# Performance work log

Measured on AMD Instinct MI355X. Metric: run time of the kernel, lower is better.

## Reference

```python
import jax, jax.numpy as jnp
import numpy as np

B, T, H = 4, 2048, 1024
NH = 16
HD = H // NH  # 64
FF = 4 * H


def setup_inputs() -> dict:
    key = jax.random.key(0)
    ks = jax.random.split(key, 11)
    s = 0.02
    return {
        "x": jax.random.normal(ks[0], (B, T, H), dtype=jnp.float32),
        "Wq": jax.random.normal(ks[1], (H, H), dtype=jnp.float32) * s,
        "bq": jnp.zeros((H,), dtype=jnp.float32),
        "Wk": jax.random.normal(ks[2], (H, H), dtype=jnp.float32) * s,
        "bk": jnp.zeros((H,), dtype=jnp.float32),
        "Wv": jax.random.normal(ks[3], (H, H), dtype=jnp.float32) * s,
        "bv": jnp.zeros((H,), dtype=jnp.float32),
        "W1": jax.random.normal(ks[4], (H, FF), dtype=jnp.float32) * s,
        "b1": jnp.zeros((FF,), dtype=jnp.float32),
        "W2": jax.random.normal(ks[5], (FF, H), dtype=jnp.float32) * s,
        "b2": jnp.zeros((H,), dtype=jnp.float32),
    }


def _block(x, Wq, bq, Wk, bk, Wv, bv, W1, b1, W2, b2):
    b, t, h = x.shape
    # multi-head masked self-attention; NOTE: scale = full h_dim ** 0.5 (as in source)
    q = (x @ Wq + bq).reshape(b, t, NH, HD).transpose(0, 2, 1, 3)  # [B,nH,T,HD]
    k = (x @ Wk + bk).reshape(b, t, NH, HD).transpose(0, 2, 1, 3)
    v = (x @ Wv + bv).reshape(b, t, NH, HD).transpose(0, 2, 1, 3)
    att = jnp.einsum("bnqd,bnkd->bnqk", q, k) / (h ** 0.5)  # [B,nH,T,T]
    causal = jnp.tril(jnp.ones((t, t), dtype=bool))
    att = jnp.where(causal, att, -jnp.inf)
    w = jax.nn.softmax(att, axis=-1)
    attn_out = jnp.einsum("bnqk,bnkd->bnqd", w, v).transpose(0, 2, 1, 3).reshape(b, t, h)
    x = x + attn_out
    # MLP (dropout p=0 -> identity)
    mlp = jax.nn.gelu(x @ W1 + b1) @ W2 + b2
    return x + mlp


def reference(x, Wq, bq, Wk, bk, Wv, bv, W1, b1, W2, b2):
    return _block(x, Wq, bq, Wk, bk, Wv, bv, W1, b1, W2, b2)
```

## Files before the change

### kernel.cpp

```cpp
#include <hip/hip_runtime.h>
#include <cstdint>
#include <cstddef>

typedef unsigned short u16;
typedef __attribute__((ext_vector_type(8))) __bf16 bf16x8;
typedef __attribute__((ext_vector_type(4))) __bf16 bf16x4;
typedef __attribute__((ext_vector_type(4))) float f32x4;
typedef __attribute__((ext_vector_type(4))) u16 u16x4;

#define MFMA(a, b, c) __builtin_amdgcn_mfma_f32_16x16x32_bf16((a), (b), (c), 0, 0, 0)

__device__ __forceinline__ u16 f2b(float f) {
  union { __bf16 h; u16 u; } v;
  v.h = (__bf16)f;
  return v.u;
}

__device__ __forceinline__ void gld16(const void* g, void* l) {
  __builtin_amdgcn_global_load_lds(
      (__attribute__((address_space(1))) void*)(void*)(g),
      (__attribute__((address_space(3))) void*)(l), 16, 0, 0);
}

__device__ __forceinline__ size_t qk_off(int t, int hd) {
  return (size_t)((((t >> 4) * 2 + (hd >> 5)) * 512)
                  + ((((hd >> 3) & 3) * 16 + (t & 15)) * 8) + (hd & 7));
}
__device__ __forceinline__ size_t v_off(int t, int hd) {
  int kk = ((t & 15) << 2) | ((t >> 4) & 3);
  return (size_t)(((t >> 6) * 4096)
                  + (((hd >> 4) * 2 + (kk >> 5)) * 512)
                  + ((((kk >> 3) & 3) * 16 + (hd & 15)) * 8) + (kk & 7));
}

__global__ void xconv(const float* __restrict__ in, u16* __restrict__ out, int n) {
  int i = (blockIdx.x * blockDim.x + threadIdx.x) * 4;
  if (i >= n) return;
  float4 v = *(const float4*)(in + i);
  u16x4 o;
  o[0] = f2b(v.x); o[1] = f2b(v.y); o[2] = f2b(v.z); o[3] = f2b(v.w);
  *(u16x4*)(out + i) = o;
}

__global__ void wtrans_all(const float* __restrict__ Wq, const float* __restrict__ Wk,
                           const float* __restrict__ Wv, const float* __restrict__ W1,
                           const float* __restrict__ W2, u16* __restrict__ Wqkvt,
                           u16* __restrict__ W1t, u16* __restrict__ W2t) {
  __shared__ float tile[32][33];
  int blk = blockIdx.x;
  const float* W;
  u16* Wt;
  int Kd, Nd, nx;
  if (blk < 3072) {
    int s = blk >> 10;
    blk &= 1023;
    W = (s == 0) ? Wq : (s == 1) ? Wk : Wv;
    Wt = Wqkvt + (size_t)s * 1048576;
    Kd = 1024; Nd = 1024; nx = 32;
  } else if (blk < 7168) {
    blk -= 3072; W = W1; Wt = W1t; Kd = 1024; Nd = 4096; nx = 128;
  } else {
    blk -= 7168; W = W2; Wt = W2t; Kd = 4096; Nd = 1024; nx = 32;
  }
  int n0 = (blk % nx) * 32, k0 = (blk / nx) * 32;
  int tx = threadIdx.x, ty = threadIdx.y;
#pragma unroll
  for (int i = 0; i < 4; i++)
    tile[ty + i * 8][tx] = W[(size_t)(k0 + ty + i * 8) * Nd + n0 + tx];
  __syncthreads();
#pragma unroll
  for (int i = 0; i < 4; i++)
    Wt[(size_t)(n0 + ty + i * 8) * Kd + k0 + tx] = f2b(tile[tx][ty + i * 8]);
}

template <int MODE, int NW>
__global__ __launch_bounds__(NW * 64) void gemm_bt(
    const u16* __restrict__ A, const u16* __restrict__ Bt,
    const float* __restrict__ b0, const float* __restrict__ b1,
    const float* __restrict__ b2, void* __restrict__ outp,
    const float* __restrict__ resid, int N, int K, float scale) {
  constexpr int NT = NW * 64;
  constexpr int NTILE = (NW == 4) ? 4 : 2;
  __shared__ __attribute__((aligned(16))) u16 As[128 * 64];
  __shared__ __attribute__((aligned(16))) u16 Bs[128 * 64];
  const int tid = threadIdx.x;
  const int wid = tid >> 6, lane = tid & 63;
  const int g = lane >> 4, r = lane & 15;
  const int bm = blockIdx.y, bn = blockIdx.x;
  const int wrow = (NW == 4) ? (wid >> 1) * 64 : (wid >> 2) * 64;
  const int wcol = (NW == 4) ? (wid & 1) * 64 : (wid & 3) * 32;

  const f32x4 zero4 = {0.f, 0.f, 0.f, 0.f};
  f32x4 acc[4][NTILE];
#pragma unroll
  for (int i = 0; i < 4; i++)
#pragma unroll
    for (int j = 0; j < NTILE; j++) acc[i][j] = zero4;

  const size_t aBase = (size_t)bm * 128 * K;
  const size_t bBase = (size_t)bn * 128 * K;
  const int ko0 = ((0 * 4 + g) ^ (r & 7)) * 8;
  const int ko1 = ((1 * 4 + g) ^ (r & 7)) * 8;

  for (int k0 = 0; k0 < K; k0 += 64) {
    __syncthreads();
#pragma unroll
    for (int i = 0; i < 2048 / NT; i++) {
      const int c0 = i * NT;
      const int cc = (c0 + tid) & 1023;
      const int row = cc >> 3;
      const int js = ((cc & 7) ^ (row & 7)) * 8;
      if (c0 < 1024)
        gld16(A + aBase + (size_t)row * K + k0 + js, As + cc * 8);
      else
        gld16(Bt + bBase + (size_t)row * K + k0 + js, Bs + cc * 8);
    }
    __syncthreads();
#pragma unroll
    for (int kh = 0; kh < 2; kh++) {
      const int ko = kh ? ko1 : ko0;
      bf16x8 af[4], bfr[NTILE];
#pragma unroll
      for (int t = 0; t < 4; t++)
        af[t] = *(const bf16x8*)&As[(wrow + t * 16 + r) * 64 + ko];
#pragma unroll
      for (int t = 0; t < NTILE; t++)
        bfr[t] = *(const bf16x8*)&Bs[(wcol + t * 16 + r) * 64 + ko];
#pragma unroll
      for (int mt = 0; mt < 4; mt++)
#pragma unroll
        for (int nt = 0; nt < NTILE; nt++)
          acc[mt][nt] = MFMA(af[mt], bfr[nt], acc[mt][nt]);
    }
  }

#pragma unroll
  for (int mt = 0; mt < 4; mt++) {
#pragma unroll
    for (int nt = 0; nt < NTILE; nt++) {
      int col = bn * 128 + wcol + nt * 16 + r;
      float bv;
      if (MODE == 4) {
        int sec = col >> 10, hcol = col & 1023;
        bv = (sec == 0) ? b0[hcol] : (sec == 1) ? b1[hcol] : b2[hcol];
      } else {
        bv = b0[col];
      }
#pragma unroll
      for (int rr = 0; rr < 4; rr++) {
        int row = bm * 128 + wrow + mt * 16 + g * 4 + rr;
        float v = acc[mt][nt][rr] + bv;
        if (MODE == 2) {
          const float c1 = -2.3025850929940457f;
          const float c2 = c1 * 0.044715f;
          float t2 = v * v;
          float z = v * (c1 + c2 * t2);
          float sg = 1.0f / (1.0f + __builtin_amdgcn_exp2f(z));
          ((u16*)outp)[(size_t)row * N + col] = f2b(v * sg);
        } else if (MODE == 3) {
          ((float*)outp)[(size_t)row * N + col] = v + resid[(size_t)row * N + col];
        } else if (MODE == 4) {
          int sec = col >> 10, hcol = col & 1023;
          int head = hcol >> 6, hd = hcol & 63;
          int bb = row >> 11, t = row & 2047;
          size_t hbase = ((size_t)bb * 16 + head) * 131072;
          u16* qout = (u16*)outp;
          if (sec == 0) {
            qout[hbase + qk_off(t, hd)] = f2b(v * scale);
          } else if (sec == 1) {
            (qout + 8388608)[hbase + qk_off(t, hd)] = f2b(v);
          } else {
            (qout + 16777216)[hbase + v_off(t, hd)] = f2b(v);
          }
        }
      }
    }
  }
}

__global__ __launch_bounds__(256) void attn_kernel(
    const u16* __restrict__ Q, const u16* __restrict__ Kc,
    const u16* __restrict__ Vt, const float* __restrict__ x,
    float* __restrict__ x1, u16* __restrict__ xb1) {
  const int bh = blockIdx.x & 63;
  const int slot = blockIdx.x >> 6;
  const int tid = threadIdx.x;
  const int wid = tid >> 6, lane = tid & 63;
  const int g = lane >> 4, c = lane & 15;
  const u16* Qh = Q + (size_t)bh * 131072;
  const u16* Kh = Kc + (size_t)bh * 131072;
  const u16* Vh = Vt + (size_t)bh * 131072;
  const int b = bh >> 4, head = bh & 15;

  __shared__ __attribute__((aligned(16))) u16 Ks[8192];
  __shared__ __attribute__((aligned(16))) u16 Vs[8192];
  __shared__ __attribute__((aligned(16))) u16 P[4][32][72];

  bf16x8 ones;
#pragma unroll
  for (int i = 0; i < 8; i++) ones[i] = (__bf16)1.0f;

  const f32x4 zero4 = {0.f, 0.f, 0.f, 0.f};

  for (int phase = 0; phase < 2; ++phase) {
    const int bt = phase ? (15 - slot) : slot;
    const int q0b = bt * 128;
    const int q0 = q0b + wid * 32;
    const int kendw = q0 + 32;
    const int nkt = bt + 1;

    bf16x8 qf[2][2];
#pragma unroll
    for (int mt = 0; mt < 2; mt++)
#pragma unroll
      for (int h = 0; h < 2; h++)
        qf[mt][h] = *(const bf16x8*)&Qh[(((q0 >> 4) + mt) * 2 + h) * 512 + lane * 8];

    f32x4 o[2][4];
    f32x4 lac[2];
#pragma unroll
    for (int mt = 0; mt < 2; mt++) {
      lac[mt] = zero4;
#pragma unroll
      for (int i = 0; i < 4; i++) o[mt][i] = zero4;
    }

    for (int kt = 0; kt < nkt; ++kt) {
      const int k0 = kt * 128;
#pragma unroll
      for (int r2 = 0; r2 < 4; r2++) {
        int idx = (r2 * 256 + tid) * 8;
        gld16(Kh + (size_t)k0 * 64 + idx, Ks + idx);
        gld16(Vh + (size_t)k0 * 64 + idx, Vs + idx);
      }
      __syncthreads();

#pragma unroll
      for (int s2 = 0; s2 < 2; ++s2) {
        const int k0s = k0 + s2 * 64;
        if (k0s < kendw) {
          bf16x8 kf[4][2], vf[4][2];
#pragma unroll
          for (int nt = 0; nt < 4; nt++)
#pragma unroll
            for (int h = 0; h < 2; h++) {
              kf[nt][h] = *(const bf16x8*)&Ks[s2 * 4096 + (nt * 2 + h) * 512 + lane * 8];
              vf[nt][h] = *(const bf16x8*)&Vs[s2 * 4096 + (nt * 2 + h) * 512 + lane * 8];
            }

          f32x4 sv[2][4];
#pragma unroll
          for (int mt = 0; mt < 2; mt++)
#pragma unroll
            for (int nt = 0; nt < 4; nt++) sv[mt][nt] = zero4;
#pragma unroll
          for (int nt = 0; nt < 4; nt++)
#pragma unroll
            for (int mt = 0; mt < 2; mt++) {
              sv[mt][nt] = MFMA(qf[mt][0], kf[nt][0], sv[mt][nt]);
              sv[mt][nt] = MFMA(qf[mt][1], kf[nt][1], sv[mt][nt]);
            }

          if (k0s + 64 > q0) {
#pragma unroll
            for (int mt = 0; mt < 2; mt++)
#pragma unroll
              for (int rr = 0; rr < 4; rr++) {
                int q = q0 + mt * 16 + g * 4 + rr;
#pragma unroll
                for (int nt = 0; nt < 4; nt++)
                  if (k0s + nt * 16 + c > q) sv[mt][nt][rr] = -1e30f;
              }
          }

#pragma unroll
          for (int mt = 0; mt < 2; mt++)
#pragma unroll
            for (int rr = 0; rr < 4; rr++) {
              union { u16x4 u; bf16x4 h; } pw;
#pragma unroll
              for (int nt = 0; nt < 4; nt++)
                pw.h[nt] = (__bf16)__builtin_amdgcn_exp2f(sv[mt][nt][rr]);
              *(u16x4*)&P[wid][mt * 16 + g * 4 + rr][4 * c] = pw.u;
            }

          asm volatile("s_waitcnt lgkmcnt(0)" ::: "memory");

#pragma unroll
          for (int mt = 0; mt < 2; mt++) {
            bf16x8 pf0 = *(const bf16x8*)&P[wid][mt * 16 + c][g * 8];
            bf16x8 pf1 = *(const bf16x8*)&P[wid][mt * 16 + c][32 + g * 8];
            lac[mt] = MFMA(pf0, ones, lac[mt]);
            lac[mt] = MFMA(pf1, ones, lac[mt]);
#pragma unroll
            for (int ot = 0; ot < 4; ot++) {
              f32x4 oo = MFMA(pf0, vf[ot][0], o[mt][ot]);
              o[mt][ot] = MFMA(pf1, vf[ot][1], oo);
            }
          }
        }
      }
      __syncthreads();
    }

    float inv[2][4];
#pragma unroll
    for (int mt = 0; mt < 2; mt++)
#pragma unroll
      for (int rr = 0; rr < 4; rr++) inv[mt][rr] = 1.0f / lac[mt][rr];
#pragma unroll
    for (int mt = 0; mt < 2; mt++)
#pragma unroll
      for (int ot = 0; ot < 4; ot++)
#pragma unroll
        for (int rr = 0; rr < 4; rr++) {
          int t = q0 + mt * 16 + g * 4 + rr;
          int hd = ot * 16 + c;
          size_t xi = ((size_t)b * 2048 + t) * 1024 + head * 64 + hd;
          float v = x[xi] + o[mt][ot][rr] * inv[mt][rr];
          x1[xi] = v;
          xb1[xi] = f2b(v);
        }
  }
}

extern "C" void kernel_launch(void* const* d_in, const int* in_sizes, int n_in,
                              void* d_out, int out_size, void* d_ws, size_t ws_size,
                              hipStream_t stream) {
  (void)in_sizes; (void)n_in; (void)out_size; (void)ws_size;
  const float* x = (const float*)d_in[0];
  const float* Wq = (const float*)d_in[1];
  const float* bq = (const float*)d_in[2];
  const float* Wk = (const float*)d_in[3];
  const float* bk = (const float*)d_in[4];
  const float* Wv = (const float*)d_in[5];
  const float* bv = (const float*)d_in[6];
  const float* W1 = (const float*)d_in[7];
  const float* b1 = (const float*)d_in[8];
  const float* W2 = (const float*)d_in[9];
  const float* b2 = (const float*)d_in[10];

  char* ws = (char*)d_ws;
  size_t off = 0;
  auto alloc = [&](size_t bytes) {
    char* p = ws + off;
    off += (bytes + 255) & ~(size_t)255;
    return p;
  };
  u16* xb    = (u16*)alloc(8192ull * 1024 * 2);
  u16* Wqkvt = (u16*)alloc(3072ull * 1024 * 2);
  u16* W1t   = (u16*)alloc(4096ull * 1024 * 2);
  u16* W2t   = (u16*)alloc(1024ull * 4096 * 2);
  u16* Qb    = (u16*)alloc(3ull * 8192 * 1024 * 2);
  float* x1  = (float*)alloc(8192ull * 1024 * 4);
  u16* hb    = (u16*)alloc(8192ull * 4096 * 2);
  u16* xb1   = xb;
  u16* Kb    = Qb + 8388608;
  u16* Vtb   = Qb + 16777216;

  const float qscale = 1.4426950408889634f / 32.0f;

  xconv<<<dim3(8192), dim3(256), 0, stream>>>(x, xb, 8192 * 1024);
  wtrans_all<<<dim3(11264), dim3(32, 8), 0, stream>>>(
      Wq, Wk, Wv, W1, W2, Wqkvt, W1t, W2t);
  gemm_bt<4, 4><<<dim3(24, 64), dim3(256), 0, stream>>>(
      xb, Wqkvt, bq, bk, bv, Qb, nullptr, 3072, 1024, qscale);
  attn_kernel<<<dim3(512), dim3(256), 0, stream>>>(Qb, Kb, Vtb, x, x1, xb1);
  gemm_bt<2, 4><<<dim3(32, 64), dim3(256), 0, stream>>>(
      xb1, W1t, b1, nullptr, nullptr, hb, nullptr, 4096, 1024, 1.0f);
  gemm_bt<3, 8><<<dim3(8, 64), dim3(512), 0, stream>>>(
      hb, W2t, b2, nullptr, nullptr, d_out, x1, 1024, 4096, 1.0f);
}
```

Measured before the change: 462.3 us.

## Add 256x256-tile double-buffered GEMM kernel for QKV and FFN1 projections

Adds a gemm256 kernel that uses 512-thread workgroups, 256x256 output tiles, double-buffered LDS loads through global_load_lds with an XOR swizzle, and an XCD-aware block remapping. It replaces the earlier gemm_bt launches for the QKV projection and the first MLP matmul. Larger tiles raise arithmetic intensity and cut global traffic. Prefetching the next K tile while the MFMAs run is meant to hide load latency. The cost is heavy register pressure from 32 accumulators per thread and 128KB of LDS per block, which may limit occupancy, and only 384 or 512 workgroups are launched.

```diff
diff --git a/kernel.cpp b/kernel.cpp
--- a/kernel.cpp
+++ b/kernel.cpp
@@ -178,6 +178,161 @@
   }
 }
 
+template <int MODE>
+__global__ __launch_bounds__(512, 2) void gemm256(
+    const u16* __restrict__ A, const u16* __restrict__ Bt,
+    const float* __restrict__ b0, const float* __restrict__ b1,
+    const float* __restrict__ b2, void* __restrict__ outp,
+    int N, int K, int nbn, float scale) {
+  __shared__ __attribute__((aligned(16))) u16 As_[2][256 * 64];
+  __shared__ __attribute__((aligned(16))) u16 Bs_[2][256 * 64];
+  const int tid = threadIdx.x;
+  const int wid = tid >> 6, lane = tid & 63;
+  const int g = lane >> 4, r = lane & 15;
+
+  const int nwg = gridDim.x;
+  const int cpx = nwg >> 3;
+  const int id2 = (blockIdx.x & 7) * cpx + (blockIdx.x >> 3);
+  const int bm = id2 / nbn, bn = id2 % nbn;
+
+  const int wrow = (wid >> 2) * 128;
+  const int wcol = (wid & 3) * 64;
+
+  const size_t aBase = (size_t)bm * 256 * K;
+  const size_t bBase = (size_t)bn * 256 * K;
+  const int ko0 = ((0 * 4 + g) ^ (r & 7)) * 8;
+  const int ko1 = ((1 * 4 + g) ^ (r & 7)) * 8;
+
+  const u16* const ab[2] = {A, Bt};
+  const size_t base2[2] = {aBase, bBase};
+
+  f32x4 acc[8][4];
+  const f32x4 zero4 = {0.f, 0.f, 0.f, 0.f};
+#pragma unroll
+  for (int i = 0; i < 8; i++)
+#pragma unroll
+    for (int j = 0; j < 4; j++) acc[i][j] = zero4;
+
+#pragma unroll
+  for (int op = 0; op < 2; op++)
+#pragma unroll
+    for (int i = 0; i < 4; i++) {
+      int cc = i * 512 + tid;
+      int row = cc >> 3;
+      int js = ((cc & 7) ^ (row & 7)) * 8;
+      gld16(ab[op] + base2[op] + (size_t)row * K + js,
+            (op ? (void*)&Bs_[0][cc * 8] : (void*)&As_[0][cc * 8]));
+    }
+  asm volatile("s_waitcnt vmcnt(0)" ::: "memory");
+  __builtin_amdgcn_s_barrier();
+
+  const int KT = K >> 6;
+  int cur = 0;
+  for (int t = 0; t < KT; ++t) {
+    const u16* as = As_[cur];
+    const u16* bs = Bs_[cur];
+    const int nxt = cur ^ 1;
+    const int knext = (t + 1) << 6;
+    const bool more = (t + 1) < KT;
+    bf16x8 af[4][2], bf[2][2];
+#pragma unroll
+    for (int mh = 0; mh < 2; mh++) {
+#pragma unroll
+      for (int nh = 0; nh < 2; nh++) {
+        if (nh == 0) {
+#pragma unroll
+          for (int mt = 0; mt < 4; mt++) {
+            int arow = wrow + mh * 64 + mt * 16 + r;
+            af[mt][0] = *(const bf16x8*)&as[arow * 64 + ko0];
+            af[mt][1] = *(const bf16x8*)&as[arow * 64 + ko1];
+          }
+        }
+#pragma unroll
+        for (int nt = 0; nt < 2; nt++) {
+          int brow = wcol + nh * 32 + nt * 16 + r;
+          bf[nt][0] = *(const bf16x8*)&bs[brow * 64 + ko0];
+          bf[nt][1] = *(const bf16x8*)&bs[brow * 64 + ko1];
+        }
+        if (mh == 0 && nh == 0 && more) {
+#pragma unroll
+          for (int i = 0; i < 4; i++) {
+            int cc = i * 512 + tid;
+            int row = cc >> 3;
+            int js = ((cc & 7) ^ (row & 7)) * 8;
+            gld16(A + aBase + (size_t)row * K + knext + js, &As_[nxt][cc * 8]);
+          }
+        }
+        if (mh == 0 && nh == 1 && more) {
+#pragma unroll
+          for (int i = 0; i < 4; i++) {
+            int cc = i * 512 + tid;
+            int row = cc >> 3;
+            int js = ((cc & 7) ^ (row & 7)) * 8;
+            gld16(Bt + bBase + (size_t)row * K + knext + js, &Bs_[nxt][cc * 8]);
+          }
+        }
+        __builtin_amdgcn_s_barrier();
+        asm volatile("s_waitcnt lgkmcnt(0)" ::: "memory");
+        __builtin_amdgcn_sched_barrier(0);
+        __builtin_amdgcn_s_setprio(1);
+#pragma unroll
+        for (int mt = 0; mt < 4; mt++)
+#pragma unroll
+          for (int nt = 0; nt < 2; nt++) {
+            f32x4 t0 = MFMA(af[mt][0], bf[nt][0], acc[mh * 4 + mt][nh * 2 + nt]);
+            acc[mh * 4 + mt][nh * 2 + nt] = MFMA(af[mt][1], bf[nt][1], t0);
+          }
+        __builtin_amdgcn_s_setprio(0);
+        if (mh == 1 && nh == 1 && more)
+          asm volatile("s_waitcnt vmcnt(0)" ::: "memory");
+        __builtin_amdgcn_s_barrier();
+      }
+    }
+    cur = nxt;
+  }
+
+#pragma unroll
+  for (int amt = 0; amt < 8; amt++) {
+#pragma unroll
+    for (int bnt = 0; bnt < 4; bnt++) {
+      int col = bn * 256 + wcol + bnt * 16 + r;
+      float bv;
+      if (MODE == 4) {
+        int sec = col >> 10, hcol = col & 1023;
+        bv = (sec == 0) ? b0[hcol] : (sec == 1) ? b1[hcol] : b2[hcol];
+      } else {
+        bv = b0[col];
+      }
+#pragma unroll
+      for (int rr = 0; rr < 4; rr++) {
+        int row = bm * 256 + wrow + amt * 16 + g * 4 + rr;
+        float v = acc[amt][bnt][rr] + bv;
+        if (MODE == 2) {
+          const float c1 = -2.3025850929940457f;
+          const float c2 = c1 * 0.044715f;
+          float t2 = v * v;
+          float z = v * (c1 + c2 * t2);
+          float sg = 1.0f / (1.0f + __builtin_amdgcn_exp2f(z));
+          ((u16*)outp)[(size_t)row * N + col] = f2b(v * sg);
+        } else if (MODE == 4) {
+          int sec = col >> 10, hcol = col & 1023;
+          int head = hcol >> 6, hd = hcol & 63;
+          int bb = row >> 11, tt = row & 2047;
+          size_t hbase = ((size_t)bb * 16 + head) * 131072;
+          u16* qout = (u16*)outp;
+          if (sec == 0) {
+            qout[hbase + qk_off(tt, hd)] = f2b(v * scale);
+          } else if (sec == 1) {
+            (qout + 8388608)[hbase + qk_off(tt, hd)] = f2b(v);
+          } else {
+            (qout + 16777216)[hbase + v_off(tt, hd)] = f2b(v);
+          }
+        }
+      }
+    }
+  }
+}
+
 __global__ __launch_bounds__(256) void attn_kernel(
     const u16* __restrict__ Q, const u16* __restrict__ Kc,
     const u16* __restrict__ Vt, const float* __restrict__ x,
@@ -363,11 +518,11 @@
   xconv<<<dim3(8192), dim3(256), 0, stream>>>(x, xb, 8192 * 1024);
   wtrans_all<<<dim3(11264), dim3(32, 8), 0, stream>>>(
       Wq, Wk, Wv, W1, W2, Wqkvt, W1t, W2t);
-  gemm_bt<4, 4><<<dim3(24, 64), dim3(256), 0, stream>>>(
-      xb, Wqkvt, bq, bk, bv, Qb, nullptr, 3072, 1024, qscale);
+  gemm256<4><<<dim3(384), dim3(512), 0, stream>>>(
+      xb, Wqkvt, bq, bk, bv, Qb, 3072, 1024, 12, qscale);
   attn_kernel<<<dim3(512), dim3(256), 0, stream>>>(Qb, Kb, Vtb, x, x1, xb1);
-  gemm_bt<2, 4><<<dim3(32, 64), dim3(256), 0, stream>>>(
-      xb1, W1t, b1, nullptr, nullptr, hb, nullptr, 4096, 1024, 1.0f);
+  gemm256<2><<<dim3(512), dim3(512), 0, stream>>>(
+      xb1, W1t, b1, nullptr, nullptr, hb, 4096, 1024, 16, 1.0f);
   gemm_bt<3, 8><<<dim3(8, 64), dim3(512), 0, stream>>>(
       hb, W2t, b2, nullptr, nullptr, d_out, x1, 1024, 4096, 1.0f);
 }
```

Measured after the change: 441.7 us. -4.5%, faster.

## Replace GEMMs with 256x128-tile triple-buffered pipelined kernel and XCD-aware block mapping

Applied to the files above, without the earlier changes.

Replaces the single-buffered 128x128 GEMM with a 256x128 tile kernel using 8 waves and a three-stage LDS ring. Global-to-LDS loads for step t+2 are interleaved with the MFMA work of step t, using explicit waitcnt, barriers and setprio to hide memory latency. Block indices are remapped so neighbouring tiles land on the same XCD, which should improve L2 reuse. In exchange, LDS use is larger (about 144KB), which may limit occupancy, and the hand-written waitcnt sequencing is fragile.

```diff
diff --git a/kernel.cpp b/kernel.cpp
--- a/kernel.cpp
+++ b/kernel.cpp
@@ -73,71 +73,127 @@
     Wt[(size_t)(n0 + ty + i * 8) * Kd + k0 + tx] = f2b(tile[tx][ty + i * 8]);
 }
 
-template <int MODE, int NW>
-__global__ __launch_bounds__(NW * 64) void gemm_bt(
+template <int MODE>
+__global__ __launch_bounds__(512, 2) void gemm256(
     const u16* __restrict__ A, const u16* __restrict__ Bt,
     const float* __restrict__ b0, const float* __restrict__ b1,
     const float* __restrict__ b2, void* __restrict__ outp,
     const float* __restrict__ resid, int N, int K, float scale) {
-  constexpr int NT = NW * 64;
-  constexpr int NTILE = (NW == 4) ? 4 : 2;
-  __shared__ __attribute__((aligned(16))) u16 As[128 * 64];
-  __shared__ __attribute__((aligned(16))) u16 Bs[128 * 64];
+  __shared__ __attribute__((aligned(16))) u16 As_[3][16384];
+  __shared__ __attribute__((aligned(16))) u16 Bs_[3][8192];
   const int tid = threadIdx.x;
   const int wid = tid >> 6, lane = tid & 63;
   const int g = lane >> 4, r = lane & 15;
-  const int bm = blockIdx.y, bn = blockIdx.x;
-  const int wrow = (NW == 4) ? (wid >> 1) * 64 : (wid >> 2) * 64;
-  const int wcol = (NW == 4) ? (wid & 1) * 64 : (wid & 3) * 32;
-
-  const f32x4 zero4 = {0.f, 0.f, 0.f, 0.f};
-  f32x4 acc[4][NTILE];
-#pragma unroll
-  for (int i = 0; i < 4; i++)
-#pragma unroll
-    for (int j = 0; j < NTILE; j++) acc[i][j] = zero4;
-
-  const size_t aBase = (size_t)bm * 128 * K;
-  const size_t bBase = (size_t)bn * 128 * K;
+
+  const int xcd = blockIdx.x & 7;
+  const int ii = blockIdx.x >> 3;
+  const int bm = xcd * 4 + ((ii & 31) >> 3);
+  const int bn = (ii >> 5) * 8 + (ii & 7);
+
+  const int wrow = (wid >> 1) * 64;
+  const int wcol = (wid & 1) * 64;
+
   const int ko0 = ((0 * 4 + g) ^ (r & 7)) * 8;
   const int ko1 = ((1 * 4 + g) ^ (r & 7)) * 8;
 
-  for (int k0 = 0; k0 < K; k0 += 64) {
-    __syncthreads();
-#pragma unroll
-    for (int i = 0; i < 2048 / NT; i++) {
-      const int c0 = i * NT;
-      const int cc = (c0 + tid) & 1023;
-      const int row = cc >> 3;
-      const int js = ((cc & 7) ^ (row & 7)) * 8;
-      if (c0 < 1024)
-        gld16(A + aBase + (size_t)row * K + k0 + js, As + cc * 8);
-      else
-        gld16(Bt + bBase + (size_t)row * K + k0 + js, Bs + cc * 8);
-    }
-    __syncthreads();
-#pragma unroll
-    for (int kh = 0; kh < 2; kh++) {
-      const int ko = kh ? ko1 : ko0;
-      bf16x8 af[4], bfr[NTILE];
-#pragma unroll
-      for (int t = 0; t < 4; t++)
-        af[t] = *(const bf16x8*)&As[(wrow + t * 16 + r) * 64 + ko];
-#pragma unroll
-      for (int t = 0; t < NTILE; t++)
-        bfr[t] = *(const bf16x8*)&Bs[(wcol + t * 16 + r) * 64 + ko];
-#pragma unroll
-      for (int mt = 0; mt < 4; mt++)
-#pragma unroll
-        for (int nt = 0; nt < NTILE; nt++)
-          acc[mt][nt] = MFMA(af[mt], bfr[nt], acc[mt][nt]);
-    }
+  size_t aOff[4], bOff[2];
+#pragma unroll
+  for (int i4 = 0; i4 < 4; i4++) {
+    int cc = i4 * 512 + tid, row = cc >> 3;
+    int js = ((cc & 7) ^ (row & 7)) * 8;
+    aOff[i4] = (size_t)(bm * 256 + row) * K + js;
+  }
+#pragma unroll
+  for (int i2 = 0; i2 < 2; i2++) {
+    int cc = i2 * 512 + tid, row = cc >> 3;
+    int js = ((cc & 7) ^ (row & 7)) * 8;
+    bOff[i2] = (size_t)(bn * 128 + row) * K + js;
+  }
+
+  f32x4 acc[4][4];
+  const f32x4 zero4 = {0.f, 0.f, 0.f, 0.f};
+#pragma unroll
+  for (int i = 0; i < 4; i++)
+#pragma unroll
+    for (int j = 0; j < 4; j++) acc[i][j] = zero4;
+
+#pragma unroll
+  for (int i4 = 0; i4 < 4; i4++) gld16(A + aOff[i4], &As_[0][(i4 * 512 + tid) * 8]);
+#pragma unroll
+  for (int i2 = 0; i2 < 2; i2++) gld16(Bt + bOff[i2], &Bs_[0][(i2 * 512 + tid) * 8]);
+#pragma unroll
+  for (int i4 = 0; i4 < 4; i4++) gld16(A + aOff[i4] + 64, &As_[1][(i4 * 512 + tid) * 8]);
+#pragma unroll
+  for (int i2 = 0; i2 < 2; i2++) gld16(Bt + bOff[i2] + 64, &Bs_[1][(i2 * 512 + tid) * 8]);
+  asm volatile("s_waitcnt vmcnt(6)" ::: "memory");
+  __builtin_amdgcn_s_barrier();
+
+  const int KT = K >> 6;
+  int cur = 0;
+  for (int t = 0; t < KT; ++t) {
+    const u16* as = As_[cur];
+    const u16* bs = Bs_[cur];
+    const int stg = (cur == 0) ? 2 : cur - 1;
+    const bool more = (t + 2) < KT;
+    const size_t k2 = (size_t)(t + 2) * 64;
+    bf16x8 af[4], bf[4];
+
+#pragma unroll
+    for (int mt = 0; mt < 4; mt++)
+      af[mt] = *(const bf16x8*)&as[(wrow + mt * 16 + r) * 64 + ko0];
+#pragma unroll
+    for (int nt = 0; nt < 4; nt++)
+      bf[nt] = *(const bf16x8*)&bs[(wcol + nt * 16 + r) * 64 + ko0];
+    if (more) {
+#pragma unroll
+      for (int i4 = 0; i4 < 4; i4++)
+        gld16(A + aOff[i4] + k2, &As_[stg][(i4 * 512 + tid) * 8]);
+    }
+    __builtin_amdgcn_s_barrier();
+    asm volatile("s_waitcnt lgkmcnt(0)" ::: "memory");
+    __builtin_amdgcn_sched_barrier(0);
+    __builtin_amdgcn_s_setprio(1);
+#pragma unroll
+    for (int mt = 0; mt < 4; mt++)
+#pragma unroll
+      for (int nt = 0; nt < 4; nt++)
+        acc[mt][nt] = MFMA(af[mt], bf[nt], acc[mt][nt]);
+    __builtin_amdgcn_s_setprio(0);
+    __builtin_amdgcn_s_barrier();
+
+#pragma unroll
+    for (int mt = 0; mt < 4; mt++)
+      af[mt] = *(const bf16x8*)&as[(wrow + mt * 16 + r) * 64 + ko1];
+#pragma unroll
+    for (int nt = 0; nt < 4; nt++)
+      bf[nt] = *(const bf16x8*)&bs[(wcol + nt * 16 + r) * 64 + ko1];
+    if (more) {
+#pragma unroll
+      for (int i2 = 0; i2 < 2; i2++)
+        gld16(Bt + bOff[i2] + k2, &Bs_[stg][(i2 * 512 + tid) * 8]);
+    }
+    __builtin_amdgcn_s_barrier();
+    asm volatile("s_waitcnt lgkmcnt(0)" ::: "memory");
+    __builtin_amdgcn_sched_barrier(0);
+    __builtin_amdgcn_s_setprio(1);
+#pragma unroll
+    for (int mt = 0; mt < 4; mt++)
+#pragma unroll
+      for (int nt = 0; nt < 4; nt++)
+        acc[mt][nt] = MFMA(af[mt], bf[nt], acc[mt][nt]);
+    __builtin_amdgcn_s_setprio(0);
+    if (t + 1 < KT) {
+      if (more) asm volatile("s_waitcnt vmcnt(6)" ::: "memory");
+      else      asm volatile("s_waitcnt vmcnt(0)" ::: "memory");
+    }
+    __builtin_amdgcn_s_barrier();
+    cur = (cur == 2) ? 0 : cur + 1;
   }
 
 #pragma unroll
   for (int mt = 0; mt < 4; mt++) {
 #pragma unroll
-    for (int nt = 0; nt < NTILE; nt++) {
+    for (int nt = 0; nt < 4; nt++) {
       int col = bn * 128 + wcol + nt * 16 + r;
       float bv;
       if (MODE == 4) {
@@ -147,9 +203,9 @@
         bv = b0[col];
       }
 #pragma unroll
-      for (int rr = 0; rr < 4; rr++) {
-        int row = bm * 128 + wrow + mt * 16 + g * 4 + rr;
-        float v = acc[mt][nt][rr] + bv;
+      for (int q = 0; q < 4; q++) {
+        int row = bm * 256 + wrow + mt * 16 + g * 4 + q;
+        float v = acc[mt][nt][q] + bv;
         if (MODE == 2) {
           const float c1 = -2.3025850929940457f;
           const float c2 = c1 * 0.044715f;
@@ -162,15 +218,15 @@
         } else if (MODE == 4) {
           int sec = col >> 10, hcol = col & 1023;
           int head = hcol >> 6, hd = hcol & 63;
-          int bb = row >> 11, t = row & 2047;
+          int bb = row >> 11, tt = row & 2047;
           size_t hbase = ((size_t)bb * 16 + head) * 131072;
           u16* qout = (u16*)outp;
           if (sec == 0) {
-            qout[hbase + qk_off(t, hd)] = f2b(v * scale);
+            qout[hbase + qk_off(tt, hd)] = f2b(v * scale);
           } else if (sec == 1) {
-            (qout + 8388608)[hbase + qk_off(t, hd)] = f2b(v);
+            (qout + 8388608)[hbase + qk_off(tt, hd)] = f2b(v);
           } else {
-            (qout + 16777216)[hbase + v_off(t, hd)] = f2b(v);
+            (qout + 16777216)[hbase + v_off(tt, hd)] = f2b(v);
           }
         }
       }
@@ -363,11 +419,11 @@
   xconv<<<dim3(8192), dim3(256), 0, stream>>>(x, xb, 8192 * 1024);
   wtrans_all<<<dim3(11264), dim3(32, 8), 0, stream>>>(
       Wq, Wk, Wv, W1, W2, Wqkvt, W1t, W2t);
-  gemm_bt<4, 4><<<dim3(24, 64), dim3(256), 0, stream>>>(
+  gemm256<4><<<dim3(768), dim3(512), 0, stream>>>(
       xb, Wqkvt, bq, bk, bv, Qb, nullptr, 3072, 1024, qscale);
   attn_kernel<<<dim3(512), dim3(256), 0, stream>>>(Qb, Kb, Vtb, x, x1, xb1);
-  gemm_bt<2, 4><<<dim3(32, 64), dim3(256), 0, stream>>>(
+  gemm256<2><<<dim3(1024), dim3(512), 0, stream>>>(
       xb1, W1t, b1, nullptr, nullptr, hb, nullptr, 4096, 1024, 1.0f);
-  gemm_bt<3, 8><<<dim3(8, 64), dim3(512), 0, stream>>>(
+  gemm256<3><<<dim3(256), dim3(512), 0, stream>>>(
       hb, W2t, b2, nullptr, nullptr, d_out, x1, 1024, 4096, 1.0f);
 }
```

After: 432.0 us. 1.07x faster.
